# Optimization experiments

Hardware: AMD Instinct MI355X
Metric: run time of the kernel (lower is better)

The kernel has to match this reference:

```python
import jax, jax.numpy as jnp
import numpy as np

EPS = 1e-5

def _conv(x, w, stride=1, padding=0):
    return jax.lax.conv_general_dilated(
        x, w, window_strides=(stride, stride),
        padding=((padding, padding), (padding, padding)),
        dimension_numbers=('NCHW', 'OIHW', 'NCHW'))

def _bn(x, gamma, beta, mean, var):
    # inference-mode batchnorm, per-channel over NCHW
    inv = gamma / jnp.sqrt(var + EPS)
    return x * inv[None, :, None, None] + (beta - mean * inv)[None, :, None, None]

def setup_inputs() -> dict:
    key = jax.random.key(0)
    ks = jax.random.split(key, 16)
    B, Cin, H, W = 64, 1024, 28, 28
    width, Cout = 256, 1024
    d = {}
    d['x'] = jax.random.normal(ks[0], (B, Cin, H, W), jnp.float32)
    d['w1'] = jax.random.normal(ks[1], (width, Cin, 1, 1), jnp.float32) * 0.03
    d['w2'] = jax.random.normal(ks[2], (width, width, 3, 3), jnp.float32) * 0.02
    d['w3'] = jax.random.normal(ks[3], (Cout, width, 1, 1), jnp.float32) * 0.03
    for i, c in [(1, width), (2, width), (3, Cout)]:
        d[f'g{i}'] = jnp.ones((c,), jnp.float32)
        d[f'b{i}'] = jnp.zeros((c,), jnp.float32)
        d[f'm{i}'] = jax.random.normal(ks[4 + i], (c,), jnp.float32) * 0.1
        d[f'v{i}'] = jax.random.uniform(ks[8 + i], (c,), jnp.float32, 0.5, 1.5)
    return d

def reference(x, w1, w2, w3, g1, b1, m1, v1, g2, b2, m2, v2, g3, b3, m3, v3):
    out = jax.nn.relu(_bn(_conv(x, w1), g1, b1, m1, v1))
    out = jax.nn.relu(_bn(_conv(out, w2, stride=1, padding=1), g2, b2, m2, v2))
    out = _bn(_conv(out, w3), g3, b3, m3, v3)
    return jax.nn.relu(out + x)
```

## Files before the change

### kernel.cpp

```cpp
#include <hip/hip_runtime.h>
#include <hip/hip_bf16.h>
#include <cstdint>
#include <cstddef>

#define EPS_BN 1e-5f
#define LDK 40
#define TILE (128 * LDK)

typedef __attribute__((ext_vector_type(8))) __bf16 bf16x8;
typedef __attribute__((ext_vector_type(4))) float f32x4;

__device__ __forceinline__ unsigned short f2b(float f) {
    __hip_bfloat16 h = __float2bfloat16(f);
    return __builtin_bit_cast(unsigned short, h);
}
__device__ __forceinline__ unsigned int pack2(float a, float b) {
    return (unsigned int)f2b(a) | ((unsigned int)f2b(b) << 16);
}
__device__ __forceinline__ void lgkm_barrier() {
    __builtin_amdgcn_s_waitcnt(0xC07F);
    __builtin_amdgcn_s_barrier();
}


__global__ void prep_bn_kernel(const float* __restrict__ g1, const float* __restrict__ b1,
                               const float* __restrict__ m1, const float* __restrict__ v1,
                               const float* __restrict__ g2, const float* __restrict__ b2,
                               const float* __restrict__ m2, const float* __restrict__ v2,
                               const float* __restrict__ g3, const float* __restrict__ b3,
                               const float* __restrict__ m3, const float* __restrict__ v3,
                               float* __restrict__ bias1, float* __restrict__ bias2,
                               float* __restrict__ bias3) {
    int t = blockIdx.x * 256 + threadIdx.x;
    if (t < 256) {
        float inv = g1[t] * rsqrtf(v1[t] + EPS_BN);
        bias1[t] = b1[t] - m1[t] * inv;
    } else if (t < 512) {
        int c = t - 256;
        float inv = g2[c] * rsqrtf(v2[c] + EPS_BN);
        bias2[c] = b2[c] - m2[c] * inv;
    } else if (t < 1536) {
        int c = t - 512;
        float inv = g3[c] * rsqrtf(v3[c] + EPS_BN);
        bias3[c] = b3[c] - m3[c] * inv;
    }
}

__global__ void repack_w1(const float* __restrict__ w1, const float* __restrict__ g1,
                          const float* __restrict__ v1, unsigned short* __restrict__ w1b) {
    int idx = blockIdx.x * 256 + threadIdx.x;
    int co = idx >> 10;
    float inv = g1[co] * rsqrtf(v1[co] + EPS_BN);
    w1b[idx] = f2b(w1[idx] * inv);
}

__global__ void repack_w2(const float* __restrict__ w2, const float* __restrict__ g2,
                          const float* __restrict__ v2, unsigned short* __restrict__ w2r) {
    int idx = blockIdx.x * 256 + threadIdx.x;
    int k9 = idx >> 16;
    int rem = idx & 65535;
    int co = rem >> 8;
    int ci = rem & 255;
    float inv = g2[co] * rsqrtf(v2[co] + EPS_BN);
    w2r[idx] = f2b(w2[(co * 256 + ci) * 9 + k9] * inv);
}

__global__ void repack_w3(const float* __restrict__ w3, const float* __restrict__ g3,
                          const float* __restrict__ v3, unsigned short* __restrict__ w3b) {
    int idx = blockIdx.x * 256 + threadIdx.x;
    int co = idx >> 8;
    float inv = g3[co] * rsqrtf(v3[co] + EPS_BN);
    w3b[idx] = f2b(w3[idx] * inv);
}

__global__ void halo_zero(unsigned short* __restrict__ in2p) {
    int idx = blockIdx.x * 256 + threadIdx.x;
    int cell = idx >> 5, l8 = idx & 31;
    int n = cell / 116, c = cell % 116;
    int h, w;
    if (c < 30)      { h = 0;      w = c; }
    else if (c < 60) { h = 29;     w = c - 30; }
    else if (c < 88) { h = c - 59; w = 0; }
    else             { h = c - 87; w = 29; }
    uint4 z = {0u, 0u, 0u, 0u};
    *reinterpret_cast<uint4*>(in2p + (((size_t)n * 900) + h * 30 + w) * 256 + l8 * 8) = z;
}

__global__ __launch_bounds__(256) void transpose_x(const float* __restrict__ x,
                                                   unsigned short* __restrict__ xt) {
    __shared__ float t[64][65];
    const int tid = threadIdx.x;
    const int sp0 = blockIdx.x * 64;
    const int c0 = blockIdx.y * 64;
    const int n = blockIdx.z;
    const float* xn = x + (size_t)n * 1024 * 784;

#pragma unroll
    for (int it = 0; it < 4; ++it) {
        int ci = it * 16 + (tid >> 4);
        int spl = (tid & 15) * 4;
        int sp = sp0 + spl;
        float4 v = {0.f, 0.f, 0.f, 0.f};
        if (sp < 784) v = *reinterpret_cast<const float4*>(xn + (size_t)(c0 + ci) * 784 + sp);
        t[ci][spl + 0] = v.x;
        t[ci][spl + 1] = v.y;
        t[ci][spl + 2] = v.z;
        t[ci][spl + 3] = v.w;
    }
    __syncthreads();

    unsigned short* xtn = xt + (size_t)n * 784 * 1024;
#pragma unroll
    for (int it = 0; it < 2; ++it) {
        int spl = it * 32 + (tid >> 3);
        int sp = sp0 + spl;
        if (sp >= 784) continue;
        int ci8 = (tid & 7) * 8;
        float v0 = t[ci8 + 0][spl], v1 = t[ci8 + 1][spl];
        float v2 = t[ci8 + 2][spl], v3 = t[ci8 + 3][spl];
        float v4 = t[ci8 + 4][spl], v5 = t[ci8 + 5][spl];
        float v6 = t[ci8 + 6][spl], v7 = t[ci8 + 7][spl];
        uint4 o = {pack2(v0, v1), pack2(v2, v3), pack2(v4, v5), pack2(v6, v7)};
        *reinterpret_cast<uint4*>(xtn + (size_t)sp * 1024 + c0 + ci8) = o;
    }
}

__device__ __forceinline__ void mfma_step(const unsigned short* As, const unsigned short* Bs,
                                          int aoff, int boff, f32x4 acc[4][4]) {
    bf16x8 a[4], b[4];
#pragma unroll
    for (int i = 0; i < 4; ++i)
        a[i] = *reinterpret_cast<const bf16x8*>(As + aoff + i * 16 * LDK);
#pragma unroll
    for (int j = 0; j < 4; ++j)
        b[j] = *reinterpret_cast<const bf16x8*>(Bs + boff + j * 16 * LDK);
#pragma unroll
    for (int i = 0; i < 4; ++i)
#pragma unroll
        for (int j = 0; j < 4; ++j)
            acc[i][j] = __builtin_amdgcn_mfma_f32_16x16x32_bf16(a[i], b[j], acc[i][j], 0, 0, 0);
}

__global__ __launch_bounds__(256) void conv1_kernel(const unsigned short* __restrict__ xt,
                                                    const unsigned short* __restrict__ w1b,
                                                    const float* __restrict__ bias1,
                                                    unsigned short* __restrict__ in2p) {
    __shared__ unsigned short As[2][TILE];
    __shared__ unsigned short Bs[2][TILE];
    const int tid = threadIdx.x;
    const int f0 = blockIdx.x * 128;
    const int m0 = blockIdx.y * 128;
    const int lane = tid & 63, wave = tid >> 6;
    const int wr = wave >> 1, wc = wave & 1;
    const int l15 = lane & 15, quad = lane >> 4;
    const int tcid = tid & 3, tcl = tid >> 2;

    const unsigned short* aptr = w1b + (size_t)(m0 + tcl) * 1024 + tcid * 8;
    const unsigned short* bptr = xt + (size_t)(f0 + tcl) * 1024 + tcid * 8;

    f32x4 acc[4][4] = {};
    const int aoff = (wr * 64 + l15) * LDK + quad * 8;
    const int boff = (wc * 64 + l15) * LDK + quad * 8;
    const int wo = tcl * LDK + tcid * 8;

    uint4 a0s0, a1s0, b0s0, b1s0, a0s1, a1s1, b0s1, b1s1;
    a0s0 = *reinterpret_cast<const uint4*>(aptr);
    a1s0 = *reinterpret_cast<const uint4*>(aptr + 65536);
    b0s0 = *reinterpret_cast<const uint4*>(bptr);
    b1s0 = *reinterpret_cast<const uint4*>(bptr + 65536);
    a0s1 = *reinterpret_cast<const uint4*>(aptr + 32);
    a1s1 = *reinterpret_cast<const uint4*>(aptr + 65536 + 32);
    b0s1 = *reinterpret_cast<const uint4*>(bptr + 32);
    b1s1 = *reinterpret_cast<const uint4*>(bptr + 65536 + 32);

    for (int kk = 0; kk < 32; kk += 2) {
        {
            unsigned short* A = As[0];
            unsigned short* B = Bs[0];
            *reinterpret_cast<uint4*>(A + wo) = a0s0;
            *reinterpret_cast<uint4*>(A + 64 * LDK + wo) = a1s0;
            *reinterpret_cast<uint4*>(B + wo) = b0s0;
            *reinterpret_cast<uint4*>(B + 64 * LDK + wo) = b1s0;
            if (kk < 30) {
                int k0 = (kk + 2) * 32;
                a0s0 = *reinterpret_cast<const uint4*>(aptr + k0);
                a1s0 = *reinterpret_cast<const uint4*>(aptr + 65536 + k0);
                b0s0 = *reinterpret_cast<const uint4*>(bptr + k0);
                b1s0 = *reinterpret_cast<const uint4*>(bptr + 65536 + k0);
            }
            lgkm_barrier();
            mfma_step(A, B, aoff, boff, acc);
        }
        {
            unsigned short* A = As[1];
            unsigned short* B = Bs[1];
            *reinterpret_cast<uint4*>(A + wo) = a0s1;
            *reinterpret_cast<uint4*>(A + 64 * LDK + wo) = a1s1;
            *reinterpret_cast<uint4*>(B + wo) = b0s1;
            *reinterpret_cast<uint4*>(B + 64 * LDK + wo) = b1s1;
            if (kk < 30) {
                int k0 = (kk + 3) * 32;
                a0s1 = *reinterpret_cast<const uint4*>(aptr + k0);
                a1s1 = *reinterpret_cast<const uint4*>(aptr + 65536 + k0);
                b0s1 = *reinterpret_cast<const uint4*>(bptr + k0);
                b1s1 = *reinterpret_cast<const uint4*>(bptr + 65536 + k0);
            }
            lgkm_barrier();
            mfma_step(A, B, aoff, boff, acc);
        }
    }

#pragma unroll
    for (int j = 0; j < 4; ++j) {
        int f = f0 + wc * 64 + j * 16 + l15;
        int n = f / 784;
        int r = f - n * 784;
        int oh = r / 28, ow = r - oh * 28;
        unsigned short* dst = in2p + ((size_t)n * 900 + (oh + 1) * 30 + (ow + 1)) * 256;
#pragma unroll
        for (int i = 0; i < 4; ++i) {
            int co = m0 + wr * 64 + i * 16 + quad * 4;
            float4 bia = *reinterpret_cast<const float4*>(bias1 + co);
            f32x4 v = acc[i][j];
            ushort4 o;
            o.x = f2b(fmaxf(v.x + bia.x, 0.f));
            o.y = f2b(fmaxf(v.y + bia.y, 0.f));
            o.z = f2b(fmaxf(v.z + bia.z, 0.f));
            o.w = f2b(fmaxf(v.w + bia.w, 0.f));
            *reinterpret_cast<ushort4*>(dst + co) = o;
        }
    }
}

__global__ __launch_bounds__(256) void conv2_kernel(const unsigned short* __restrict__ in2p,
                                                    const unsigned short* __restrict__ w2r,
                                                    const float* __restrict__ bias2,
                                                    unsigned short* __restrict__ in3) {
    __shared__ unsigned short As[2][TILE];
    __shared__ unsigned short Bs[2][TILE];
    const int tid = threadIdx.x;
    const int f0 = blockIdx.x * 128;
    const int m0 = blockIdx.y * 128;
    const int lane = tid & 63, wave = tid >> 6;
    const int wr = wave >> 1, wc = wave & 1;
    const int l15 = lane & 15, quad = lane >> 4;
    const int tcid = tid & 3, tcl = tid >> 2;

    int cellc[2];
#pragma unroll
    for (int p = 0; p < 2; ++p) {
        int f = f0 + p * 64 + tcl;
        int n = f / 784;
        int r = f - n * 784;
        int oh = r / 28, ow = r - oh * 28;
        cellc[p] = n * 900 + (oh + 1) * 30 + (ow + 1);
    }

    f32x4 acc[4][4] = {};
    const int aoff = (wr * 64 + l15) * LDK + quad * 8;
    const int boff = (wc * 64 + l15) * LDK + quad * 8;
    const int wo = tcl * LDK + tcid * 8;

    uint4 a0s0, a1s0, b0s0, b1s0, a0s1, a1s1, b0s1, b1s1;
    {
        a0s0 = *reinterpret_cast<const uint4*>(w2r + (size_t)(m0 + tcl) * 256 + tcid * 8);
        a1s0 = *reinterpret_cast<const uint4*>(w2r + (size_t)(m0 + 64 + tcl) * 256 + tcid * 8);
        b0s0 = *reinterpret_cast<const uint4*>(in2p + (size_t)(cellc[0] - 31) * 256 + tcid * 8);
        b1s0 = *reinterpret_cast<const uint4*>(in2p + (size_t)(cellc[1] - 31) * 256 + tcid * 8);
    }
    {
        const unsigned short* wb = w2r + 32;
        a0s1 = *reinterpret_cast<const uint4*>(wb + (size_t)(m0 + tcl) * 256 + tcid * 8);
        a1s1 = *reinterpret_cast<const uint4*>(wb + (size_t)(m0 + 64 + tcl) * 256 + tcid * 8);
        const unsigned short* bb = in2p + 32 + tcid * 8;
        b0s1 = *reinterpret_cast<const uint4*>(bb + (size_t)(cellc[0] - 31) * 256);
        b1s1 = *reinterpret_cast<const uint4*>(bb + (size_t)(cellc[1] - 31) * 256);
    }

    for (int kk = 0; kk < 72; kk += 2) {
        {
            unsigned short* A = As[0];
            unsigned short* B = Bs[0];
            *reinterpret_cast<uint4*>(A + wo) = a0s0;
            *reinterpret_cast<uint4*>(A + 64 * LDK + wo) = a1s0;
            *reinterpret_cast<uint4*>(B + wo) = b0s0;
            *reinterpret_cast<uint4*>(B + 64 * LDK + wo) = b1s0;
            if (kk < 70) {
                int kn = kk + 2;
                int k9 = kn >> 3, cb = kn & 7;
                int kh = k9 / 3, kw = k9 - 3 * kh;
                int dd = (kh - 1) * 30 + (kw - 1);
                const unsigned short* wb = w2r + (size_t)k9 * 65536 + cb * 32;
                a0s0 = *reinterpret_cast<const uint4*>(wb + (size_t)(m0 + tcl) * 256 + tcid * 8);
                a1s0 = *reinterpret_cast<const uint4*>(wb + (size_t)(m0 + 64 + tcl) * 256 + tcid * 8);
                const unsigned short* bb = in2p + (size_t)cb * 32 + tcid * 8;
                b0s0 = *reinterpret_cast<const uint4*>(bb + (size_t)(cellc[0] + dd) * 256);
                b1s0 = *reinterpret_cast<const uint4*>(bb + (size_t)(cellc[1] + dd) * 256);
            }
            lgkm_barrier();
            mfma_step(A, B, aoff, boff, acc);
        }
        {
            unsigned short* A = As[1];
            unsigned short* B = Bs[1];
            *reinterpret_cast<uint4*>(A + wo) = a0s1;
            *reinterpret_cast<uint4*>(A + 64 * LDK + wo) = a1s1;
            *reinterpret_cast<uint4*>(B + wo) = b0s1;
            *reinterpret_cast<uint4*>(B + 64 * LDK + wo) = b1s1;
            if (kk < 70) {
                int kn = kk + 3;
                int k9 = kn >> 3, cb = kn & 7;
                int kh = k9 / 3, kw = k9 - 3 * kh;
                int dd = (kh - 1) * 30 + (kw - 1);
                const unsigned short* wb = w2r + (size_t)k9 * 65536 + cb * 32;
                a0s1 = *reinterpret_cast<const uint4*>(wb + (size_t)(m0 + tcl) * 256 + tcid * 8);
                a1s1 = *reinterpret_cast<const uint4*>(wb + (size_t)(m0 + 64 + tcl) * 256 + tcid * 8);
                const unsigned short* bb = in2p + (size_t)cb * 32 + tcid * 8;
                b0s1 = *reinterpret_cast<const uint4*>(bb + (size_t)(cellc[0] + dd) * 256);
                b1s1 = *reinterpret_cast<const uint4*>(bb + (size_t)(cellc[1] + dd) * 256);
            }
            lgkm_barrier();
            mfma_step(A, B, aoff, boff, acc);
        }
    }

#pragma unroll
    for (int j = 0; j < 4; ++j) {
        int f = f0 + wc * 64 + j * 16 + l15;
        unsigned short* dst = in3 + (size_t)f * 256;
#pragma unroll
        for (int i = 0; i < 4; ++i) {
            int co = m0 + wr * 64 + i * 16 + quad * 4;
            float4 bia = *reinterpret_cast<const float4*>(bias2 + co);
            f32x4 v = acc[i][j];
            ushort4 o;
            o.x = f2b(fmaxf(v.x + bia.x, 0.f));
            o.y = f2b(fmaxf(v.y + bia.y, 0.f));
            o.z = f2b(fmaxf(v.z + bia.z, 0.f));
            o.w = f2b(fmaxf(v.w + bia.w, 0.f));
            *reinterpret_cast<ushort4*>(dst + co) = o;
        }
    }
}

__global__ __launch_bounds__(256) void conv3_kernel(const unsigned short* __restrict__ in3,
                                                    const unsigned short* __restrict__ w3b,
                                                    const float* __restrict__ bias3,
                                                    const float* __restrict__ x,
                                                    float* __restrict__ out) {
    __shared__ unsigned short As[2][TILE];
    __shared__ unsigned short Bs[2][TILE];
    const int tid = threadIdx.x;
    const int f0 = blockIdx.x * 128;
    const int m0 = blockIdx.y * 128;
    const int lane = tid & 63, wave = tid >> 6;
    const int wr = wave >> 1, wc = wave & 1;
    const int l15 = lane & 15, quad = lane >> 4;
    const int tcid = tid & 3, tcl = tid >> 2;

    const unsigned short* aptr = in3 + (size_t)(f0 + tcl) * 256 + tcid * 8;
    const unsigned short* bptr = w3b + (size_t)(m0 + tcl) * 256 + tcid * 8;

    const int aoff = (wr * 64 + l15) * LDK + quad * 8;
    const int boff = (wc * 64 + l15) * LDK + quad * 8;
    const int wo = tcl * LDK + tcid * 8;

    uint4 ra0, ra1, rb0, rb1;
    ra0 = *reinterpret_cast<const uint4*>(aptr);
    ra1 = *reinterpret_cast<const uint4*>(aptr + 16384);
    rb0 = *reinterpret_cast<const uint4*>(bptr);
    rb1 = *reinterpret_cast<const uint4*>(bptr + 16384);

    f32x4 acc[4][4];
#pragma unroll
    for (int j = 0; j < 4; ++j) {
        int co = m0 + wc * 64 + j * 16 + l15;
        float b = bias3[co];
#pragma unroll
        for (int i = 0; i < 4; ++i) {
            int fb = f0 + wr * 64 + i * 16 + quad * 4;
            int n = fb / 784;
            int sp = fb - n * 784;
            float4 xr = *reinterpret_cast<const float4*>(x + ((size_t)n * 1024 + co) * 784 + sp);
            f32x4 a;
            a.x = xr.x + b;
            a.y = xr.y + b;
            a.z = xr.z + b;
            a.w = xr.w + b;
            acc[i][j] = a;
        }
    }

    for (int kk = 0; kk < 8; ++kk) {
        unsigned short* A = As[kk & 1];
        unsigned short* B = Bs[kk & 1];
        *reinterpret_cast<uint4*>(A + wo) = ra0;
        *reinterpret_cast<uint4*>(A + 64 * LDK + wo) = ra1;
        *reinterpret_cast<uint4*>(B + wo) = rb0;
        *reinterpret_cast<uint4*>(B + 64 * LDK + wo) = rb1;
        if (kk < 7) {
            int k0 = (kk + 1) * 32;
            ra0 = *reinterpret_cast<const uint4*>(aptr + k0);
            ra1 = *reinterpret_cast<const uint4*>(aptr + 16384 + k0);
            rb0 = *reinterpret_cast<const uint4*>(bptr + k0);
            rb1 = *reinterpret_cast<const uint4*>(bptr + 16384 + k0);
        }
        lgkm_barrier();
        mfma_step(A, B, aoff, boff, acc);
    }

#pragma unroll
    for (int j = 0; j < 4; ++j) {
        int co = m0 + wc * 64 + j * 16 + l15;
#pragma unroll
        for (int i = 0; i < 4; ++i) {
            int fb = f0 + wr * 64 + i * 16 + quad * 4;
            int n = fb / 784;
            int sp = fb - n * 784;
            size_t off = ((size_t)n * 1024 + co) * 784 + sp;
            f32x4 v = acc[i][j];
            float4 o;
            o.x = fmaxf(v.x, 0.f);
            o.y = fmaxf(v.y, 0.f);
            o.z = fmaxf(v.z, 0.f);
            o.w = fmaxf(v.w, 0.f);
            *reinterpret_cast<float4*>(out + off) = o;
        }
    }
}


extern "C" void kernel_launch(void* const* d_in, const int* in_sizes, int n_in,
                              void* d_out, int out_size, void* d_ws, size_t ws_size,
                              hipStream_t stream) {
    const float* x  = (const float*)d_in[0];
    const float* w1 = (const float*)d_in[1];
    const float* w2 = (const float*)d_in[2];
    const float* w3 = (const float*)d_in[3];
    const float* g1 = (const float*)d_in[4];
    const float* b1 = (const float*)d_in[5];
    const float* m1 = (const float*)d_in[6];
    const float* v1 = (const float*)d_in[7];
    const float* g2 = (const float*)d_in[8];
    const float* b2 = (const float*)d_in[9];
    const float* m2 = (const float*)d_in[10];
    const float* v2 = (const float*)d_in[11];
    const float* g3 = (const float*)d_in[12];
    const float* b3 = (const float*)d_in[13];
    const float* m3 = (const float*)d_in[14];
    const float* v3 = (const float*)d_in[15];

    char* ws = (char*)d_ws;
    unsigned short* w1b  = (unsigned short*)(ws + 0);
    unsigned short* w2r  = (unsigned short*)(ws + 524288);
    unsigned short* w3b  = (unsigned short*)(ws + 1703936);
    float* bias1         = (float*)(ws + 2228224);
    float* bias2         = (float*)(ws + 2229248);
    float* bias3         = (float*)(ws + 2230272);
    unsigned short* in2p = (unsigned short*)(ws + 2234368);
    unsigned short* xt   = (unsigned short*)(ws + 31725568);
    unsigned short* in3  = xt;

    prep_bn_kernel<<<6, 256, 0, stream>>>(g1, b1, m1, v1, g2, b2, m2, v2, g3, b3, m3, v3,
                                          bias1, bias2, bias3);
    repack_w1<<<1024, 256, 0, stream>>>(w1, g1, v1, w1b);
    repack_w2<<<2304, 256, 0, stream>>>(w2, g2, v2, w2r);
    repack_w3<<<1024, 256, 0, stream>>>(w3, g3, v3, w3b);
    halo_zero<<<928, 256, 0, stream>>>(in2p);

    transpose_x<<<dim3(13, 16, 64), 256, 0, stream>>>(x, xt);
    conv1_kernel<<<dim3(392, 2), 256, 0, stream>>>(xt, w1b, bias1, in2p);
    conv2_kernel<<<dim3(392, 2), 256, 0, stream>>>(in2p, w2r, bias2, in3);
    conv3_kernel<<<dim3(392, 8), 256, 0, stream>>>(in3, w3b, bias3, x, (float*)d_out);
}
```

Baseline: 646.7 us.

## Load conv3 MFMA operands directly from global memory, skipping LDS staging

The conv3 GEMM no longer stages A/B tiles through double-buffered shared memory with barriers. Each wave now loads its bf16x8 MFMA fragments straight from global memory (K=256 is small) with a fully unrolled k-loop. The grid is also transposed so the 8 output-channel blocks sharing an activation tile are adjacent, which should improve L2 reuse of in3. The cost is redundant global/L2 fragment loads across waves and less coalesced 16-byte accesses in exchange for removing LDS writes and syncs.

```diff
diff --git a/kernel.cpp b/kernel.cpp
--- a/kernel.cpp
+++ b/kernel.cpp
@@ -348,28 +348,15 @@
                                                     const float* __restrict__ bias3,
                                                     const float* __restrict__ x,
                                                     float* __restrict__ out) {
-    __shared__ unsigned short As[2][TILE];
-    __shared__ unsigned short Bs[2][TILE];
     const int tid = threadIdx.x;
-    const int f0 = blockIdx.x * 128;
-    const int m0 = blockIdx.y * 128;
+    const int m0 = blockIdx.x * 128;
+    const int f0 = blockIdx.y * 128;
     const int lane = tid & 63, wave = tid >> 6;
     const int wr = wave >> 1, wc = wave & 1;
     const int l15 = lane & 15, quad = lane >> 4;
-    const int tcid = tid & 3, tcl = tid >> 2;
-
-    const unsigned short* aptr = in3 + (size_t)(f0 + tcl) * 256 + tcid * 8;
-    const unsigned short* bptr = w3b + (size_t)(m0 + tcl) * 256 + tcid * 8;
-
-    const int aoff = (wr * 64 + l15) * LDK + quad * 8;
-    const int boff = (wc * 64 + l15) * LDK + quad * 8;
-    const int wo = tcl * LDK + tcid * 8;
-
-    uint4 ra0, ra1, rb0, rb1;
-    ra0 = *reinterpret_cast<const uint4*>(aptr);
-    ra1 = *reinterpret_cast<const uint4*>(aptr + 16384);
-    rb0 = *reinterpret_cast<const uint4*>(bptr);
-    rb1 = *reinterpret_cast<const uint4*>(bptr + 16384);
+
+    const unsigned short* abase = in3 + (size_t)(f0 + wr * 64 + l15) * 256 + quad * 8;
+    const unsigned short* bbase = w3b + (size_t)(m0 + wc * 64 + l15) * 256 + quad * 8;
 
     f32x4 acc[4][4];
 #pragma unroll
@@ -391,22 +378,20 @@
         }
     }
 
+#pragma unroll
     for (int kk = 0; kk < 8; ++kk) {
-        unsigned short* A = As[kk & 1];
-        unsigned short* B = Bs[kk & 1];
-        *reinterpret_cast<uint4*>(A + wo) = ra0;
-        *reinterpret_cast<uint4*>(A + 64 * LDK + wo) = ra1;
-        *reinterpret_cast<uint4*>(B + wo) = rb0;
-        *reinterpret_cast<uint4*>(B + 64 * LDK + wo) = rb1;
-        if (kk < 7) {
-            int k0 = (kk + 1) * 32;
-            ra0 = *reinterpret_cast<const uint4*>(aptr + k0);
-            ra1 = *reinterpret_cast<const uint4*>(aptr + 16384 + k0);
-            rb0 = *reinterpret_cast<const uint4*>(bptr + k0);
-            rb1 = *reinterpret_cast<const uint4*>(bptr + 16384 + k0);
-        }
-        lgkm_barrier();
-        mfma_step(A, B, aoff, boff, acc);
+        bf16x8 a[4], b[4];
+#pragma unroll
+        for (int i = 0; i < 4; ++i)
+            a[i] = *reinterpret_cast<const bf16x8*>(abase + i * 16 * 256 + kk * 32);
+#pragma unroll
+        for (int j = 0; j < 4; ++j)
+            b[j] = *reinterpret_cast<const bf16x8*>(bbase + j * 16 * 256 + kk * 32);
+#pragma unroll
+        for (int i = 0; i < 4; ++i)
+#pragma unroll
+            for (int j = 0; j < 4; ++j)
+                acc[i][j] = __builtin_amdgcn_mfma_f32_16x16x32_bf16(a[i], b[j], acc[i][j], 0, 0, 0);
     }
 
 #pragma unroll
@@ -471,5 +456,5 @@
     transpose_x<<<dim3(13, 16, 64), 256, 0, stream>>>(x, xt);
     conv1_kernel<<<dim3(392, 2), 256, 0, stream>>>(xt, w1b, bias1, in2p);
     conv2_kernel<<<dim3(392, 2), 256, 0, stream>>>(in2p, w2r, bias2, in3);
-    conv3_kernel<<<dim3(392, 8), 256, 0, stream>>>(in3, w3b, bias3, x, (float*)d_out);
-}
+    conv3_kernel<<<dim3(8, 392), 256, 0, stream>>>(in3, w3b, bias3, x, (float*)d_out);
+}
```

New measurement: 682.8 us. 5.6% more time.

## Use direct global-to-LDS loads with triple buffering in conv2

Applied to the files above, without the earlier changes.

Rewrites the conv2 implicit-GEMM main loop to use global_load_lds, so tiles go straight from global memory into LDS without passing through registers. It adds a three-stage LDS ring with vmcnt-based barriers to keep two tiles in flight. The LDS row pitch drops from the padded 40 to an unpadded 32 elements, which the direct-to-LDS layout needs. That removes the bank-conflict padding, so the MFMA fragment reads may hit more LDS bank conflicts.

```diff
diff --git a/kernel.cpp b/kernel.cpp
--- a/kernel.cpp
+++ b/kernel.cpp
@@ -4,8 +4,8 @@
 #include <cstddef>
 
 #define EPS_BN 1e-5f
-#define LDK 40
-#define TILE (128 * LDK)
+#define LDK1 40
+#define TILE1 (128 * LDK1)
 
 typedef __attribute__((ext_vector_type(8))) __bf16 bf16x8;
 typedef __attribute__((ext_vector_type(4))) float f32x4;
@@ -20,6 +20,15 @@
 __device__ __forceinline__ void lgkm_barrier() {
     __builtin_amdgcn_s_waitcnt(0xC07F);
     __builtin_amdgcn_s_barrier();
+}
+#define VM_BARRIER(N) do { \
+        __builtin_amdgcn_s_waitcnt(0x3F70 | (N)); \
+        __builtin_amdgcn_s_barrier(); \
+    } while (0)
+__device__ __forceinline__ void load_lds16(const unsigned short* g, unsigned short* l) {
+    __builtin_amdgcn_global_load_lds(
+        (__attribute__((address_space(1))) void*)g,
+        (__attribute__((address_space(3))) void*)l, 16, 0, 0);
 }
 
 
@@ -126,14 +135,14 @@
 }
 
 __device__ __forceinline__ void mfma_step(const unsigned short* As, const unsigned short* Bs,
-                                          int aoff, int boff, f32x4 acc[4][4]) {
+                                          int aoff, int boff, int ld, f32x4 acc[4][4]) {
     bf16x8 a[4], b[4];
 #pragma unroll
     for (int i = 0; i < 4; ++i)
-        a[i] = *reinterpret_cast<const bf16x8*>(As + aoff + i * 16 * LDK);
+        a[i] = *reinterpret_cast<const bf16x8*>(As + aoff + i * 16 * ld);
 #pragma unroll
     for (int j = 0; j < 4; ++j)
-        b[j] = *reinterpret_cast<const bf16x8*>(Bs + boff + j * 16 * LDK);
+        b[j] = *reinterpret_cast<const bf16x8*>(Bs + boff + j * 16 * ld);
 #pragma unroll
     for (int i = 0; i < 4; ++i)
 #pragma unroll
@@ -145,8 +154,8 @@
                                                     const unsigned short* __restrict__ w1b,
                                                     const float* __restrict__ bias1,
                                                     unsigned short* __restrict__ in2p) {
-    __shared__ unsigned short As[2][TILE];
-    __shared__ unsigned short Bs[2][TILE];
+    __shared__ unsigned short As[2][TILE1];
+    __shared__ unsigned short Bs[2][TILE1];
     const int tid = threadIdx.x;
     const int f0 = blockIdx.x * 128;
     const int m0 = blockIdx.y * 128;
@@ -159,9 +168,9 @@
     const unsigned short* bptr = xt + (size_t)(f0 + tcl) * 1024 + tcid * 8;
 
     f32x4 acc[4][4] = {};
-    const int aoff = (wr * 64 + l15) * LDK + quad * 8;
-    const int boff = (wc * 64 + l15) * LDK + quad * 8;
-    const int wo = tcl * LDK + tcid * 8;
+    const int aoff = (wr * 64 + l15) * LDK1 + quad * 8;
+    const int boff = (wc * 64 + l15) * LDK1 + quad * 8;
+    const int wo = tcl * LDK1 + tcid * 8;
 
     uint4 a0s0, a1s0, b0s0, b1s0, a0s1, a1s1, b0s1, b1s1;
     a0s0 = *reinterpret_cast<const uint4*>(aptr);
@@ -178,9 +187,9 @@
             unsigned short* A = As[0];
             unsigned short* B = Bs[0];
             *reinterpret_cast<uint4*>(A + wo) = a0s0;
-            *reinterpret_cast<uint4*>(A + 64 * LDK + wo) = a1s0;
+            *reinterpret_cast<uint4*>(A + 64 * LDK1 + wo) = a1s0;
             *reinterpret_cast<uint4*>(B + wo) = b0s0;
-            *reinterpret_cast<uint4*>(B + 64 * LDK + wo) = b1s0;
+            *reinterpret_cast<uint4*>(B + 64 * LDK1 + wo) = b1s0;
             if (kk < 30) {
                 int k0 = (kk + 2) * 32;
                 a0s0 = *reinterpret_cast<const uint4*>(aptr + k0);
@@ -189,15 +198,15 @@
                 b1s0 = *reinterpret_cast<const uint4*>(bptr + 65536 + k0);
             }
             lgkm_barrier();
-            mfma_step(A, B, aoff, boff, acc);
+            mfma_step(A, B, aoff, boff, LDK1, acc);
         }
         {
             unsigned short* A = As[1];
             unsigned short* B = Bs[1];
             *reinterpret_cast<uint4*>(A + wo) = a0s1;
-            *reinterpret_cast<uint4*>(A + 64 * LDK + wo) = a1s1;
+            *reinterpret_cast<uint4*>(A + 64 * LDK1 + wo) = a1s1;
             *reinterpret_cast<uint4*>(B + wo) = b0s1;
-            *reinterpret_cast<uint4*>(B + 64 * LDK + wo) = b1s1;
+            *reinterpret_cast<uint4*>(B + 64 * LDK1 + wo) = b1s1;
             if (kk < 30) {
                 int k0 = (kk + 3) * 32;
                 a0s1 = *reinterpret_cast<const uint4*>(aptr + k0);
@@ -206,7 +215,7 @@
                 b1s1 = *reinterpret_cast<const uint4*>(bptr + 65536 + k0);
             }
             lgkm_barrier();
-            mfma_step(A, B, aoff, boff, acc);
+            mfma_step(A, B, aoff, boff, LDK1, acc);
         }
     }
 
@@ -236,93 +245,62 @@
                                                     const unsigned short* __restrict__ w2r,
                                                     const float* __restrict__ bias2,
                                                     unsigned short* __restrict__ in3) {
-    __shared__ unsigned short As[2][TILE];
-    __shared__ unsigned short Bs[2][TILE];
+    __shared__ unsigned short As[3][4096];
+    __shared__ unsigned short Bs[3][4096];
     const int tid = threadIdx.x;
     const int f0 = blockIdx.x * 128;
     const int m0 = blockIdx.y * 128;
     const int lane = tid & 63, wave = tid >> 6;
     const int wr = wave >> 1, wc = wave & 1;
     const int l15 = lane & 15, quad = lane >> 4;
-    const int tcid = tid & 3, tcl = tid >> 2;
-
-    int cellc[2];
+    const int srow = wave * 16 + (lane >> 2);
+    const int scol8 = (lane & 3) * 8;
+    const int lso = wave * 512;
+
+    int cellr[2];
 #pragma unroll
     for (int p = 0; p < 2; ++p) {
-        int f = f0 + p * 64 + tcl;
+        int f = f0 + p * 64 + srow;
         int n = f / 784;
         int r = f - n * 784;
         int oh = r / 28, ow = r - oh * 28;
-        cellc[p] = n * 900 + (oh + 1) * 30 + (ow + 1);
-    }
+        cellr[p] = n * 900 + (oh + 1) * 30 + (ow + 1);
+    }
+
+    const unsigned short* wbase = w2r + (size_t)(m0 + srow) * 256 + scol8;
 
     f32x4 acc[4][4] = {};
-    const int aoff = (wr * 64 + l15) * LDK + quad * 8;
-    const int boff = (wc * 64 + l15) * LDK + quad * 8;
-    const int wo = tcl * LDK + tcid * 8;
-
-    uint4 a0s0, a1s0, b0s0, b1s0, a0s1, a1s1, b0s1, b1s1;
-    {
-        a0s0 = *reinterpret_cast<const uint4*>(w2r + (size_t)(m0 + tcl) * 256 + tcid * 8);
-        a1s0 = *reinterpret_cast<const uint4*>(w2r + (size_t)(m0 + 64 + tcl) * 256 + tcid * 8);
-        b0s0 = *reinterpret_cast<const uint4*>(in2p + (size_t)(cellc[0] - 31) * 256 + tcid * 8);
-        b1s0 = *reinterpret_cast<const uint4*>(in2p + (size_t)(cellc[1] - 31) * 256 + tcid * 8);
-    }
-    {
-        const unsigned short* wb = w2r + 32;
-        a0s1 = *reinterpret_cast<const uint4*>(wb + (size_t)(m0 + tcl) * 256 + tcid * 8);
-        a1s1 = *reinterpret_cast<const uint4*>(wb + (size_t)(m0 + 64 + tcl) * 256 + tcid * 8);
-        const unsigned short* bb = in2p + 32 + tcid * 8;
-        b0s1 = *reinterpret_cast<const uint4*>(bb + (size_t)(cellc[0] - 31) * 256);
-        b1s1 = *reinterpret_cast<const uint4*>(bb + (size_t)(cellc[1] - 31) * 256);
-    }
-
-    for (int kk = 0; kk < 72; kk += 2) {
-        {
-            unsigned short* A = As[0];
-            unsigned short* B = Bs[0];
-            *reinterpret_cast<uint4*>(A + wo) = a0s0;
-            *reinterpret_cast<uint4*>(A + 64 * LDK + wo) = a1s0;
-            *reinterpret_cast<uint4*>(B + wo) = b0s0;
-            *reinterpret_cast<uint4*>(B + 64 * LDK + wo) = b1s0;
-            if (kk < 70) {
-                int kn = kk + 2;
-                int k9 = kn >> 3, cb = kn & 7;
-                int kh = k9 / 3, kw = k9 - 3 * kh;
-                int dd = (kh - 1) * 30 + (kw - 1);
-                const unsigned short* wb = w2r + (size_t)k9 * 65536 + cb * 32;
-                a0s0 = *reinterpret_cast<const uint4*>(wb + (size_t)(m0 + tcl) * 256 + tcid * 8);
-                a1s0 = *reinterpret_cast<const uint4*>(wb + (size_t)(m0 + 64 + tcl) * 256 + tcid * 8);
-                const unsigned short* bb = in2p + (size_t)cb * 32 + tcid * 8;
-                b0s0 = *reinterpret_cast<const uint4*>(bb + (size_t)(cellc[0] + dd) * 256);
-                b1s0 = *reinterpret_cast<const uint4*>(bb + (size_t)(cellc[1] + dd) * 256);
-            }
-            lgkm_barrier();
-            mfma_step(A, B, aoff, boff, acc);
-        }
-        {
-            unsigned short* A = As[1];
-            unsigned short* B = Bs[1];
-            *reinterpret_cast<uint4*>(A + wo) = a0s1;
-            *reinterpret_cast<uint4*>(A + 64 * LDK + wo) = a1s1;
-            *reinterpret_cast<uint4*>(B + wo) = b0s1;
-            *reinterpret_cast<uint4*>(B + 64 * LDK + wo) = b1s1;
-            if (kk < 70) {
-                int kn = kk + 3;
-                int k9 = kn >> 3, cb = kn & 7;
-                int kh = k9 / 3, kw = k9 - 3 * kh;
-                int dd = (kh - 1) * 30 + (kw - 1);
-                const unsigned short* wb = w2r + (size_t)k9 * 65536 + cb * 32;
-                a0s1 = *reinterpret_cast<const uint4*>(wb + (size_t)(m0 + tcl) * 256 + tcid * 8);
-                a1s1 = *reinterpret_cast<const uint4*>(wb + (size_t)(m0 + 64 + tcl) * 256 + tcid * 8);
-                const unsigned short* bb = in2p + (size_t)cb * 32 + tcid * 8;
-                b0s1 = *reinterpret_cast<const uint4*>(bb + (size_t)(cellc[0] + dd) * 256);
-                b1s1 = *reinterpret_cast<const uint4*>(bb + (size_t)(cellc[1] + dd) * 256);
-            }
-            lgkm_barrier();
-            mfma_step(A, B, aoff, boff, acc);
-        }
-    }
+    const int aoff = (wr * 64 + l15) * 32 + quad * 8;
+    const int boff = (wc * 64 + l15) * 32 + quad * 8;
+
+#define STAGE2(cur, kn) do { \
+        int k9_ = (kn) >> 3, cb_ = (kn) & 7; \
+        int kh_ = k9_ / 3, kw_ = k9_ - 3 * kh_; \
+        int dd_ = (kh_ - 1) * 30 + (kw_ - 1); \
+        const unsigned short* wa_ = wbase + (size_t)k9_ * 65536 + cb_ * 32; \
+        load_lds16(wa_, &As[cur][lso]); \
+        load_lds16(wa_ + 16384, &As[cur][lso + 2048]); \
+        const unsigned short* bb_ = in2p + (size_t)cb_ * 32 + scol8; \
+        load_lds16(bb_ + (size_t)(cellr[0] + dd_) * 256, &Bs[cur][lso]); \
+        load_lds16(bb_ + (size_t)(cellr[1] + dd_) * 256, &Bs[cur][lso + 2048]); \
+    } while (0)
+
+    STAGE2(0, 0);
+    STAGE2(1, 1);
+    for (int kk = 0; kk < 72; ++kk) {
+        int cur = kk % 3;
+        if (kk < 70) {
+            STAGE2((kk + 2) % 3, kk + 2);
+            VM_BARRIER(8);
+        } else if (kk == 70) {
+            VM_BARRIER(4);
+        } else {
+            VM_BARRIER(0);
+        }
+        mfma_step(As[cur], Bs[cur], aoff, boff, 32, acc);
+        __builtin_amdgcn_s_barrier();
+    }
+#undef STAGE2
 
 #pragma unroll
     for (int j = 0; j < 4; ++j) {
@@ -348,8 +326,8 @@
                                                     const float* __restrict__ bias3,
                                                     const float* __restrict__ x,
                                                     float* __restrict__ out) {
-    __shared__ unsigned short As[2][TILE];
-    __shared__ unsigned short Bs[2][TILE];
+    __shared__ unsigned short As[2][TILE1];
+    __shared__ unsigned short Bs[2][TILE1];
     const int tid = threadIdx.x;
     const int f0 = blockIdx.x * 128;
     const int m0 = blockIdx.y * 128;
@@ -361,9 +339,9 @@
     const unsigned short* aptr = in3 + (size_t)(f0 + tcl) * 256 + tcid * 8;
     const unsigned short* bptr = w3b + (size_t)(m0 + tcl) * 256 + tcid * 8;
 
-    const int aoff = (wr * 64 + l15) * LDK + quad * 8;
-    const int boff = (wc * 64 + l15) * LDK + quad * 8;
-    const int wo = tcl * LDK + tcid * 8;
+    const int aoff = (wr * 64 + l15) * LDK1 + quad * 8;
+    const int boff = (wc * 64 + l15) * LDK1 + quad * 8;
+    const int wo = tcl * LDK1 + tcid * 8;
 
     uint4 ra0, ra1, rb0, rb1;
     ra0 = *reinterpret_cast<const uint4*>(aptr);
@@ -395,9 +373,9 @@
         unsigned short* A = As[kk & 1];
         unsigned short* B = Bs[kk & 1];
         *reinterpret_cast<uint4*>(A + wo) = ra0;
-        *reinterpret_cast<uint4*>(A + 64 * LDK + wo) = ra1;
+        *reinterpret_cast<uint4*>(A + 64 * LDK1 + wo) = ra1;
         *reinterpret_cast<uint4*>(B + wo) = rb0;
-        *reinterpret_cast<uint4*>(B + 64 * LDK + wo) = rb1;
+        *reinterpret_cast<uint4*>(B + 64 * LDK1 + wo) = rb1;
         if (kk < 7) {
             int k0 = (kk + 1) * 32;
             ra0 = *reinterpret_cast<const uint4*>(aptr + k0);
@@ -406,7 +384,7 @@
             rb1 = *reinterpret_cast<const uint4*>(bptr + 16384 + k0);
         }
         lgkm_barrier();
-        mfma_step(A, B, aoff, boff, acc);
+        mfma_step(A, B, aoff, boff, LDK1, acc);
     }
 
 #pragma unroll
```

Measured after the change: 655.5 us. Within noise of the previous version (+1.4%).

## Fuse input transpose/bf16 cast into conv1 and widen block to all 256 channels

Applied to the files above, without the earlier changes.

Removes the separate transpose_x kernel and has conv1 read fp32 NCHW x directly, converting pairs of channels to bf16 while staging the B tile in shared memory. conv1 now uses 512-thread blocks covering all 256 output channels per 128-pixel tile, so x is read once rather than once per output-channel block. This saves the bf16 transposed copy's write and re-read, but the x loads are now scalar, strided by 784 floats per channel, and the LDS B stores are 4-byte rather than 16-byte, which may reduce load efficiency.

```diff
diff --git a/kernel.cpp b/kernel.cpp
--- a/kernel.cpp
+++ b/kernel.cpp
@@ -4,8 +4,8 @@
 #include <cstddef>
 
 #define EPS_BN 1e-5f
-#define LDK 40
-#define TILE (128 * LDK)
+#define LDK1 40
+#define TILE1 (128 * LDK1)
 
 typedef __attribute__((ext_vector_type(8))) __bf16 bf16x8;
 typedef __attribute__((ext_vector_type(4))) float f32x4;
@@ -86,54 +86,15 @@
     *reinterpret_cast<uint4*>(in2p + (((size_t)n * 900) + h * 30 + w) * 256 + l8 * 8) = z;
 }
 
-__global__ __launch_bounds__(256) void transpose_x(const float* __restrict__ x,
-                                                   unsigned short* __restrict__ xt) {
-    __shared__ float t[64][65];
-    const int tid = threadIdx.x;
-    const int sp0 = blockIdx.x * 64;
-    const int c0 = blockIdx.y * 64;
-    const int n = blockIdx.z;
-    const float* xn = x + (size_t)n * 1024 * 784;
-
-#pragma unroll
-    for (int it = 0; it < 4; ++it) {
-        int ci = it * 16 + (tid >> 4);
-        int spl = (tid & 15) * 4;
-        int sp = sp0 + spl;
-        float4 v = {0.f, 0.f, 0.f, 0.f};
-        if (sp < 784) v = *reinterpret_cast<const float4*>(xn + (size_t)(c0 + ci) * 784 + sp);
-        t[ci][spl + 0] = v.x;
-        t[ci][spl + 1] = v.y;
-        t[ci][spl + 2] = v.z;
-        t[ci][spl + 3] = v.w;
-    }
-    __syncthreads();
-
-    unsigned short* xtn = xt + (size_t)n * 784 * 1024;
-#pragma unroll
-    for (int it = 0; it < 2; ++it) {
-        int spl = it * 32 + (tid >> 3);
-        int sp = sp0 + spl;
-        if (sp >= 784) continue;
-        int ci8 = (tid & 7) * 8;
-        float v0 = t[ci8 + 0][spl], v1 = t[ci8 + 1][spl];
-        float v2 = t[ci8 + 2][spl], v3 = t[ci8 + 3][spl];
-        float v4 = t[ci8 + 4][spl], v5 = t[ci8 + 5][spl];
-        float v6 = t[ci8 + 6][spl], v7 = t[ci8 + 7][spl];
-        uint4 o = {pack2(v0, v1), pack2(v2, v3), pack2(v4, v5), pack2(v6, v7)};
-        *reinterpret_cast<uint4*>(xtn + (size_t)sp * 1024 + c0 + ci8) = o;
-    }
-}
-
 __device__ __forceinline__ void mfma_step(const unsigned short* As, const unsigned short* Bs,
-                                          int aoff, int boff, f32x4 acc[4][4]) {
+                                          int aoff, int boff, int ld, f32x4 acc[4][4]) {
     bf16x8 a[4], b[4];
 #pragma unroll
     for (int i = 0; i < 4; ++i)
-        a[i] = *reinterpret_cast<const bf16x8*>(As + aoff + i * 16 * LDK);
+        a[i] = *reinterpret_cast<const bf16x8*>(As + aoff + i * 16 * ld);
 #pragma unroll
     for (int j = 0; j < 4; ++j)
-        b[j] = *reinterpret_cast<const bf16x8*>(Bs + boff + j * 16 * LDK);
+        b[j] = *reinterpret_cast<const bf16x8*>(Bs + boff + j * 16 * ld);
 #pragma unroll
     for (int i = 0; i < 4; ++i)
 #pragma unroll
@@ -141,85 +102,75 @@
             acc[i][j] = __builtin_amdgcn_mfma_f32_16x16x32_bf16(a[i], b[j], acc[i][j], 0, 0, 0);
 }
 
-__global__ __launch_bounds__(256) void conv1_kernel(const unsigned short* __restrict__ xt,
+__global__ __launch_bounds__(512) void conv1_kernel(const float* __restrict__ x,
                                                     const unsigned short* __restrict__ w1b,
                                                     const float* __restrict__ bias1,
                                                     unsigned short* __restrict__ in2p) {
-    __shared__ unsigned short As[2][TILE];
-    __shared__ unsigned short Bs[2][TILE];
+    __shared__ unsigned short As[2][256 * LDK1];
+    __shared__ unsigned short Bs[2][128 * LDK1];
     const int tid = threadIdx.x;
     const int f0 = blockIdx.x * 128;
-    const int m0 = blockIdx.y * 128;
     const int lane = tid & 63, wave = tid >> 6;
-    const int wr = wave >> 1, wc = wave & 1;
+    const int wA = wave & 3;
+    const int wB = wave >> 2;
     const int l15 = lane & 15, quad = lane >> 4;
-    const int tcid = tid & 3, tcl = tid >> 2;
-
-    const unsigned short* aptr = w1b + (size_t)(m0 + tcl) * 1024 + tcid * 8;
-    const unsigned short* bptr = xt + (size_t)(f0 + tcl) * 1024 + tcid * 8;
+
+    const int ar = tid >> 1, ah = (tid & 1) * 16;
+    const unsigned short* aptr = w1b + (size_t)ar * 1024 + ah;
+    const int awo = ar * LDK1 + ah;
+
+    const int cp = tid >> 5, sq = tid & 31;
+    const float* xb[4];
+    int bwo[4];
+#pragma unroll
+    for (int e = 0; e < 4; ++e) {
+        int f = f0 + sq + 32 * e;
+        int n = f / 784, sp = f - n * 784;
+        xb[e] = x + ((size_t)n * 1024 + 2 * cp) * 784 + sp;
+        bwo[e] = (sq + 32 * e) * LDK1 + 2 * cp;
+    }
 
     f32x4 acc[4][4] = {};
-    const int aoff = (wr * 64 + l15) * LDK + quad * 8;
-    const int boff = (wc * 64 + l15) * LDK + quad * 8;
-    const int wo = tcl * LDK + tcid * 8;
-
-    uint4 a0s0, a1s0, b0s0, b1s0, a0s1, a1s1, b0s1, b1s1;
-    a0s0 = *reinterpret_cast<const uint4*>(aptr);
-    a1s0 = *reinterpret_cast<const uint4*>(aptr + 65536);
-    b0s0 = *reinterpret_cast<const uint4*>(bptr);
-    b1s0 = *reinterpret_cast<const uint4*>(bptr + 65536);
-    a0s1 = *reinterpret_cast<const uint4*>(aptr + 32);
-    a1s1 = *reinterpret_cast<const uint4*>(aptr + 65536 + 32);
-    b0s1 = *reinterpret_cast<const uint4*>(bptr + 32);
-    b1s1 = *reinterpret_cast<const uint4*>(bptr + 65536 + 32);
-
-    for (int kk = 0; kk < 32; kk += 2) {
-        {
-            unsigned short* A = As[0];
-            unsigned short* B = Bs[0];
-            *reinterpret_cast<uint4*>(A + wo) = a0s0;
-            *reinterpret_cast<uint4*>(A + 64 * LDK + wo) = a1s0;
-            *reinterpret_cast<uint4*>(B + wo) = b0s0;
-            *reinterpret_cast<uint4*>(B + 64 * LDK + wo) = b1s0;
-            if (kk < 30) {
-                int k0 = (kk + 2) * 32;
-                a0s0 = *reinterpret_cast<const uint4*>(aptr + k0);
-                a1s0 = *reinterpret_cast<const uint4*>(aptr + 65536 + k0);
-                b0s0 = *reinterpret_cast<const uint4*>(bptr + k0);
-                b1s0 = *reinterpret_cast<const uint4*>(bptr + 65536 + k0);
-            }
-            lgkm_barrier();
-            mfma_step(A, B, aoff, boff, acc);
-        }
-        {
-            unsigned short* A = As[1];
-            unsigned short* B = Bs[1];
-            *reinterpret_cast<uint4*>(A + wo) = a0s1;
-            *reinterpret_cast<uint4*>(A + 64 * LDK + wo) = a1s1;
-            *reinterpret_cast<uint4*>(B + wo) = b0s1;
-            *reinterpret_cast<uint4*>(B + 64 * LDK + wo) = b1s1;
-            if (kk < 30) {
-                int k0 = (kk + 3) * 32;
-                a0s1 = *reinterpret_cast<const uint4*>(aptr + k0);
-                a1s1 = *reinterpret_cast<const uint4*>(aptr + 65536 + k0);
-                b0s1 = *reinterpret_cast<const uint4*>(bptr + k0);
-                b1s1 = *reinterpret_cast<const uint4*>(bptr + 65536 + k0);
-            }
-            lgkm_barrier();
-            mfma_step(A, B, aoff, boff, acc);
-        }
+    const int aoff = (wA * 64 + l15) * LDK1 + quad * 8;
+    const int boff = (wB * 64 + l15) * LDK1 + quad * 8;
+
+    uint4 ra0, ra1;
+    float bv0[4], bv1[4];
+    ra0 = *reinterpret_cast<const uint4*>(aptr);
+    ra1 = *reinterpret_cast<const uint4*>(aptr + 8);
+#pragma unroll
+    for (int e = 0; e < 4; ++e) { bv0[e] = xb[e][0]; bv1[e] = xb[e][784]; }
+
+    for (int kk = 0; kk < 32; ++kk) {
+        unsigned short* A = As[kk & 1];
+        unsigned short* B = Bs[kk & 1];
+        *reinterpret_cast<uint4*>(A + awo) = ra0;
+        *reinterpret_cast<uint4*>(A + awo + 8) = ra1;
+#pragma unroll
+        for (int e = 0; e < 4; ++e)
+            *reinterpret_cast<unsigned int*>(B + bwo[e]) = pack2(bv0[e], bv1[e]);
+        if (kk < 31) {
+            int ka = (kk + 1) * 32;
+            ra0 = *reinterpret_cast<const uint4*>(aptr + ka);
+            ra1 = *reinterpret_cast<const uint4*>(aptr + ka + 8);
+            size_t kb = (size_t)(kk + 1) * 32 * 784;
+#pragma unroll
+            for (int e = 0; e < 4; ++e) { bv0[e] = xb[e][kb]; bv1[e] = xb[e][kb + 784]; }
+        }
+        lgkm_barrier();
+        mfma_step(A, B, aoff, boff, LDK1, acc);
     }
 
 #pragma unroll
     for (int j = 0; j < 4; ++j) {
-        int f = f0 + wc * 64 + j * 16 + l15;
+        int f = f0 + wB * 64 + j * 16 + l15;
         int n = f / 784;
         int r = f - n * 784;
         int oh = r / 28, ow = r - oh * 28;
         unsigned short* dst = in2p + ((size_t)n * 900 + (oh + 1) * 30 + (ow + 1)) * 256;
 #pragma unroll
         for (int i = 0; i < 4; ++i) {
-            int co = m0 + wr * 64 + i * 16 + quad * 4;
+            int co = wA * 64 + i * 16 + quad * 4;
             float4 bia = *reinterpret_cast<const float4*>(bias1 + co);
             f32x4 v = acc[i][j];
             ushort4 o;
@@ -236,8 +187,8 @@
                                                     const unsigned short* __restrict__ w2r,
                                                     const float* __restrict__ bias2,
                                                     unsigned short* __restrict__ in3) {
-    __shared__ unsigned short As[2][TILE];
-    __shared__ unsigned short Bs[2][TILE];
+    __shared__ unsigned short As[2][TILE1];
+    __shared__ unsigned short Bs[2][TILE1];
     const int tid = threadIdx.x;
     const int f0 = blockIdx.x * 128;
     const int m0 = blockIdx.y * 128;
@@ -257,9 +208,9 @@
     }
 
     f32x4 acc[4][4] = {};
-    const int aoff = (wr * 64 + l15) * LDK + quad * 8;
-    const int boff = (wc * 64 + l15) * LDK + quad * 8;
-    const int wo = tcl * LDK + tcid * 8;
+    const int aoff = (wr * 64 + l15) * LDK1 + quad * 8;
+    const int boff = (wc * 64 + l15) * LDK1 + quad * 8;
+    const int wo = tcl * LDK1 + tcid * 8;
 
     uint4 a0s0, a1s0, b0s0, b1s0, a0s1, a1s1, b0s1, b1s1;
     {
@@ -282,9 +233,9 @@
             unsigned short* A = As[0];
             unsigned short* B = Bs[0];
             *reinterpret_cast<uint4*>(A + wo) = a0s0;
-            *reinterpret_cast<uint4*>(A + 64 * LDK + wo) = a1s0;
+            *reinterpret_cast<uint4*>(A + 64 * LDK1 + wo) = a1s0;
             *reinterpret_cast<uint4*>(B + wo) = b0s0;
-            *reinterpret_cast<uint4*>(B + 64 * LDK + wo) = b1s0;
+            *reinterpret_cast<uint4*>(B + 64 * LDK1 + wo) = b1s0;
             if (kk < 70) {
                 int kn = kk + 2;
                 int k9 = kn >> 3, cb = kn & 7;
@@ -298,15 +249,15 @@
                 b1s0 = *reinterpret_cast<const uint4*>(bb + (size_t)(cellc[1] + dd) * 256);
             }
             lgkm_barrier();
-            mfma_step(A, B, aoff, boff, acc);
+            mfma_step(A, B, aoff, boff, LDK1, acc);
         }
         {
             unsigned short* A = As[1];
             unsigned short* B = Bs[1];
             *reinterpret_cast<uint4*>(A + wo) = a0s1;
-            *reinterpret_cast<uint4*>(A + 64 * LDK + wo) = a1s1;
+            *reinterpret_cast<uint4*>(A + 64 * LDK1 + wo) = a1s1;
             *reinterpret_cast<uint4*>(B + wo) = b0s1;
-            *reinterpret_cast<uint4*>(B + 64 * LDK + wo) = b1s1;
+            *reinterpret_cast<uint4*>(B + 64 * LDK1 + wo) = b1s1;
             if (kk < 70) {
                 int kn = kk + 3;
                 int k9 = kn >> 3, cb = kn & 7;
@@ -320,7 +271,7 @@
                 b1s1 = *reinterpret_cast<const uint4*>(bb + (size_t)(cellc[1] + dd) * 256);
             }
             lgkm_barrier();
-            mfma_step(A, B, aoff, boff, acc);
+            mfma_step(A, B, aoff, boff, LDK1, acc);
         }
     }
 
@@ -348,8 +299,8 @@
                                                     const float* __restrict__ bias3,
                                                     const float* __restrict__ x,
                                                     float* __restrict__ out) {
-    __shared__ unsigned short As[2][TILE];
-    __shared__ unsigned short Bs[2][TILE];
+    __shared__ unsigned short As[2][TILE1];
+    __shared__ unsigned short Bs[2][TILE1];
     const int tid = threadIdx.x;
     const int f0 = blockIdx.x * 128;
     const int m0 = blockIdx.y * 128;
@@ -361,9 +312,9 @@
     const unsigned short* aptr = in3 + (size_t)(f0 + tcl) * 256 + tcid * 8;
     const unsigned short* bptr = w3b + (size_t)(m0 + tcl) * 256 + tcid * 8;
 
-    const int aoff = (wr * 64 + l15) * LDK + quad * 8;
-    const int boff = (wc * 64 + l15) * LDK + quad * 8;
-    const int wo = tcl * LDK + tcid * 8;
+    const int aoff = (wr * 64 + l15) * LDK1 + quad * 8;
+    const int boff = (wc * 64 + l15) * LDK1 + quad * 8;
+    const int wo = tcl * LDK1 + tcid * 8;
 
     uint4 ra0, ra1, rb0, rb1;
     ra0 = *reinterpret_cast<const uint4*>(aptr);
@@ -395,9 +346,9 @@
         unsigned short* A = As[kk & 1];
         unsigned short* B = Bs[kk & 1];
         *reinterpret_cast<uint4*>(A + wo) = ra0;
-        *reinterpret_cast<uint4*>(A + 64 * LDK + wo) = ra1;
+        *reinterpret_cast<uint4*>(A + 64 * LDK1 + wo) = ra1;
         *reinterpret_cast<uint4*>(B + wo) = rb0;
-        *reinterpret_cast<uint4*>(B + 64 * LDK + wo) = rb1;
+        *reinterpret_cast<uint4*>(B + 64 * LDK1 + wo) = rb1;
         if (kk < 7) {
             int k0 = (kk + 1) * 32;
             ra0 = *reinterpret_cast<const uint4*>(aptr + k0);
@@ -406,7 +357,7 @@
             rb1 = *reinterpret_cast<const uint4*>(bptr + 16384 + k0);
         }
         lgkm_barrier();
-        mfma_step(A, B, aoff, boff, acc);
+        mfma_step(A, B, aoff, boff, LDK1, acc);
     }
 
 #pragma unroll
@@ -458,8 +409,7 @@
     float* bias2         = (float*)(ws + 2229248);
     float* bias3         = (float*)(ws + 2230272);
     unsigned short* in2p = (unsigned short*)(ws + 2234368);
-    unsigned short* xt   = (unsigned short*)(ws + 31725568);
-    unsigned short* in3  = xt;
+    unsigned short* in3  = (unsigned short*)(ws + 31725568);
 
     prep_bn_kernel<<<6, 256, 0, stream>>>(g1, b1, m1, v1, g2, b2, m2, v2, g3, b3, m3, v3,
                                           bias1, bias2, bias3);
@@ -468,8 +418,7 @@
     repack_w3<<<1024, 256, 0, stream>>>(w3, g3, v3, w3b);
     halo_zero<<<928, 256, 0, stream>>>(in2p);
 
-    transpose_x<<<dim3(13, 16, 64), 256, 0, stream>>>(x, xt);
-    conv1_kernel<<<dim3(392, 2), 256, 0, stream>>>(xt, w1b, bias1, in2p);
+    conv1_kernel<<<dim3(392), 512, 0, stream>>>(x, w1b, bias1, in2p);
     conv2_kernel<<<dim3(392, 2), 256, 0, stream>>>(in2p, w2r, bias2, in3);
     conv3_kernel<<<dim3(392, 8), 256, 0, stream>>>(in3, w3b, bias3, x, (float*)d_out);
 }
```

Measured after the change: 591.7 us. 8.5% less time.
